# Optimization experiments

Measured on AMD Instinct MI355X. Metric: run time of the kernel, lower is better.

## Reference

```python
import jax, jax.numpy as jnp
import numpy as np

EPS = 1e-12

def _l2_normalize(v, axis):
    norm = jnp.linalg.norm(v, ord=2, axis=axis, keepdims=True)
    return v / jnp.maximum(norm, EPS)

def setup_inputs() -> dict:
    key = jax.random.key(0)
    k1, k2, k3 = jax.random.split(key, 3)
    B, H, W, D, K = 16, 56, 56, 512, 32
    x = jax.random.normal(k1, (B, H, W, D), dtype=jnp.float32)
    # 1x1 conv weight (no bias): equivalent to a (D,K) matmul; he_normal-ish scale
    Wc = jax.random.normal(k2, (D, K), dtype=jnp.float32) * jnp.sqrt(2.0 / D)
    # cluster centers, original shape (1,1,1,512,32) -> stored as (D,K)
    C = jax.random.normal(k3, (D, K), dtype=jnp.float32) * jnp.sqrt(2.0 / D)
    return {"x": x, "Wc": Wc, "C": C}

def reference(x, Wc, C):
    # soft-assignment: 1x1 conv + softmax over clusters
    s = jnp.einsum('bhwd,dk->bhwk', x, Wc)          # (B,H,W,K)
    a = jax.nn.softmax(s, axis=-1)                   # (B,H,W,K)
    # v[b,d,k] = sum_{h,w} a[b,h,w,k] * (x[b,h,w,d] + C[d,k])
    #          = einsum(a,x) + C * sum_{h,w} a   (avoids (B,H,W,D,K) intermediate)
    ax = jnp.einsum('bhwk,bhwd->bdk', a, x)          # (B,D,K)
    a_sum = jnp.sum(a, axis=(1, 2))                  # (B,K)
    v = ax + C[None, :, :] * a_sum[:, None, :]       # (B,D,K)
    # intra-normalize over cluster axis (dim=2), flatten, L2 normalize
    v = _l2_normalize(v, axis=2)
    v = v.reshape(v.shape[0], -1)                    # (B, D*K)
    return _l2_normalize(v, axis=1)
```

## Files before the change

### kernel.cpp

```cpp
#include <hip/hip_runtime.h>
#include <math.h>


#define BATCH 16
#define HW    3136
#define DIM   512
#define KCL   32
#define NCHK  49
#define SLABF (BATCH * DIM * KCL + 256)

typedef __attribute__((ext_vector_type(8))) short short8;
typedef __attribute__((ext_vector_type(4))) float f32x4;

__device__ __forceinline__ void atomAddF(float* p, float v) {
    unsafeAtomicAdd(p, v);
}

__device__ __forceinline__ unsigned short f2bf(float f) {
    unsigned u = __float_as_uint(f);
    return (unsigned short)((u + 0x7FFFu + ((u >> 16) & 1u)) >> 16);
}

__device__ __forceinline__ short8 pack_frag(f32x4 lo, f32x4 hi) {
    union { unsigned short h[8]; short8 s; } r;
    r.h[0] = f2bf(lo[0]); r.h[1] = f2bf(lo[1]); r.h[2] = f2bf(lo[2]); r.h[3] = f2bf(lo[3]);
    r.h[4] = f2bf(hi[0]); r.h[5] = f2bf(hi[1]); r.h[6] = f2bf(hi[2]); r.h[7] = f2bf(hi[3]);
    return r.s;
}

__device__ __forceinline__ f32x4 gload4(const float* p) {
    f32x4 r;
    asm volatile("global_load_dwordx4 %0, %1, off" : "=v"(r) : "v"(p) : "memory");
    return r;
}
__device__ __forceinline__ float gload1(const float* p) {
    float r;
    asm volatile("global_load_dword %0, %1, off" : "=v"(r) : "v"(p) : "memory");
    return r;
}

#define WAITV(N)                                                               \
    do {                                                                       \
        asm volatile("s_waitcnt vmcnt(" #N ")" ::: "memory");                  \
        __builtin_amdgcn_sched_barrier(0);                                     \
    } while (0)

#define WT_STR 520
#define AT_STR 72
#define XT_STR 72

#define P1_TAIL(C, N)                                                          \
    {                                                                          \
        asm volatile("s_waitcnt vmcnt(" #N ")" ::: "memory");                  \
        __builtin_amdgcn_sched_barrier(0);                                     \
        short8 af = pack_frag(afb[(C) & 7][0], afb[(C) & 7][1]);               \
        short8 b0 = *(const short8*)&wt[l15 * WT_STR + (C) * 32 + quad * 8];   \
        short8 b1 = *(const short8*)&wt[(16 + l15) * WT_STR + (C) * 32 + quad * 8]; \
        acc0 = __builtin_amdgcn_mfma_f32_16x16x32_bf16(af, b0, acc0, 0, 0, 0); \
        acc1 = __builtin_amdgcn_mfma_f32_16x16x32_bf16(af, b1, acc1, 0, 0, 0); \
    }

#define LOAD_PF_ASM(PF, DC)                                                    \
    _Pragma("unroll")                                                          \
    for (int i = 0; i < 8; ++i) {                                              \
        const int p = (ph + 2 * i) * 4;                                        \
        _Pragma("unroll")                                                      \
        for (int j = 0; j < 4; ++j)                                            \
            PF[i * 4 + j] = gload1(xc + (size_t)(p + j) * DIM + (DC));         \
    }

#define P2_STAGE(PF)                                                           \
    _Pragma("unroll")                                                          \
    for (int i = 0; i < 8; ++i) {                                              \
        const int p = (ph + 2 * i) * 4;                                        \
        ushort4 w;                                                             \
        w.x = f2bf(PF[i * 4 + 0]); w.y = f2bf(PF[i * 4 + 1]);                  \
        w.z = f2bf(PF[i * 4 + 2]); w.w = f2bf(PF[i * 4 + 3]);                  \
        *(ushort4*)&xt[xtrow * XT_STR + (p ^ xsw)] = w;                        \
    }

#define P2_MFMA_STORE(DC)                                                      \
    {                                                                          \
        f32x4 z = {0.f, 0.f, 0.f, 0.f};                                        \
        f32x4 pacc[2][2];                                                      \
        pacc[0][0] = z; pacc[0][1] = z; pacc[1][0] = z; pacc[1][1] = z;        \
        _Pragma("unroll")                                                      \
        for (int s_ = 0; s_ < 2; ++s_) {                                       \
            const int pb = s_ * 32 + quad * 8;                                 \
            short8 bf0 = *(const short8*)&aT[l15 * AT_STR + pb];               \
            short8 bf1 = *(const short8*)&aT[(16 + l15) * AT_STR + pb];        \
            _Pragma("unroll")                                                  \
            for (int m2 = 0; m2 < 2; ++m2) {                                   \
                const int dloc = wv * 32 + m2 * 16 + l15;                      \
                short8 af = *(const short8*)&xt[dloc * XT_STR + (pb ^ (((dloc >> 3) & 7) << 3))]; \
                pacc[m2][0] = __builtin_amdgcn_mfma_f32_16x16x32_bf16(af, bf0, pacc[m2][0], 0, 0, 0); \
                pacc[m2][1] = __builtin_amdgcn_mfma_f32_16x16x32_bf16(af, bf1, pacc[m2][1], 0, 0, 0); \
            }                                                                  \
        }                                                                      \
        _Pragma("unroll")                                                      \
        for (int m2 = 0; m2 < 2; ++m2) {                                       \
            const int dr = (DC) + (wv * 2 + m2) * 16 + quad * 4;               \
            _Pragma("unroll")                                                  \
            for (int r = 0; r < 4; ++r) {                                      \
                vp[(size_t)(dr + r) * KCL + l15]      = pacc[m2][0][r];        \
                vp[(size_t)(dr + r) * KCL + 16 + l15] = pacc[m2][1][r];        \
            }                                                                  \
        }                                                                      \
    }

__global__ __launch_bounds__(256, 3) void k_sax(const float* __restrict__ x,
                                                const float* __restrict__ Wc,
                                                float* __restrict__ vpart,
                                                float* __restrict__ a_sum) {
    __shared__ __align__(16) unsigned short wt[32 * WT_STR];
    __shared__ __align__(16) unsigned short aT[KCL * AT_STR];
    __shared__ float asum_l[4][32];
    const int t    = threadIdx.x;
    const int lane = t & 63;
    const int wv   = t >> 6;
    const int l15  = lane & 15;
    const int quad = lane >> 4;
    const int n0   = blockIdx.x * 64;
    const int b    = n0 / HW;
    const int ch   = blockIdx.x % NCHK;

    const float* xr = x + (size_t)(n0 + wv * 16 + l15) * DIM + quad * 8;

    f32x4 afb[8][2];
#pragma unroll
    for (int c = 0; c < 8; ++c) {
        afb[c][0] = gload4(xr + c * 32);
        afb[c][1] = gload4(xr + c * 32 + 4);
    }

#pragma unroll
    for (int i = 0; i < 16; ++i) {
        int f  = i * 256 + t;
        int d  = f >> 3;
        int k4 = (f & 7) * 4;
        float4 v = *(const float4*)(Wc + (size_t)d * KCL + k4);
        wt[(k4 + 0) * WT_STR + d] = f2bf(v.x);
        wt[(k4 + 1) * WT_STR + d] = f2bf(v.y);
        wt[(k4 + 2) * WT_STR + d] = f2bf(v.z);
        wt[(k4 + 3) * WT_STR + d] = f2bf(v.w);
    }
    __syncthreads();
    WAITV(0);

    f32x4 acc0 = {0.f, 0.f, 0.f, 0.f};
    f32x4 acc1 = {0.f, 0.f, 0.f, 0.f};
#pragma unroll
    for (int c = 0; c < 8; ++c) {
        short8 af = pack_frag(afb[c][0], afb[c][1]);
        afb[c][0] = gload4(xr + (c + 8) * 32);
        afb[c][1] = gload4(xr + (c + 8) * 32 + 4);
        short8 b0 = *(const short8*)&wt[l15 * WT_STR + c * 32 + quad * 8];
        short8 b1 = *(const short8*)&wt[(16 + l15) * WT_STR + c * 32 + quad * 8];
        acc0 = __builtin_amdgcn_mfma_f32_16x16x32_bf16(af, b0, acc0, 0, 0, 0);
        acc1 = __builtin_amdgcn_mfma_f32_16x16x32_bf16(af, b1, acc1, 0, 0, 0);
    }
    P1_TAIL(8, 14)  P1_TAIL(9, 12)  P1_TAIL(10, 10) P1_TAIL(11, 8)
    P1_TAIL(12, 6)  P1_TAIL(13, 4)  P1_TAIL(14, 2)  P1_TAIL(15, 0)

    float at0 = 0.f, at1 = 0.f;
#pragma unroll
    for (int r = 0; r < 4; ++r) {
        float m = fmaxf(acc0[r], acc1[r]);
        m = fmaxf(m, __shfl_xor(m, 1));
        m = fmaxf(m, __shfl_xor(m, 2));
        m = fmaxf(m, __shfl_xor(m, 4));
        m = fmaxf(m, __shfl_xor(m, 8));
        float e0 = __expf(acc0[r] - m);
        float e1 = __expf(acc1[r] - m);
        float s = e0 + e1;
        s += __shfl_xor(s, 1);
        s += __shfl_xor(s, 2);
        s += __shfl_xor(s, 4);
        s += __shfl_xor(s, 8);
        float inv = 1.f / s;
        float a0 = e0 * inv, a1 = e1 * inv;
        const int pos = wv * 16 + quad * 4 + r;
        aT[l15 * AT_STR + pos]        = f2bf(a0);
        aT[(16 + l15) * AT_STR + pos] = f2bf(a1);
        at0 += a0; at1 += a1;
    }
    at0 += __shfl_xor(at0, 16); at0 += __shfl_xor(at0, 32);
    at1 += __shfl_xor(at1, 16); at1 += __shfl_xor(at1, 32);
    if (quad == 0) {
        asum_l[wv][l15]      = at0;
        asum_l[wv][16 + l15] = at1;
    }

    const int rw    = lane & 31;
    const int ph    = lane >> 5;
    const int xtrow = wv * 32 + rw;
    const int xsw   = ((xtrow >> 3) & 7) << 3;
    unsigned short* xt = wt;
    const float* xc = x + (size_t)n0 * DIM + xtrow;
    float* vp = vpart + (size_t)ch * SLABF + (size_t)b * DIM * KCL;

    float pfA[32], pfB[32];
    LOAD_PF_ASM(pfA, 0);

    __syncthreads();

    WAITV(0);
    LOAD_PF_ASM(pfB, 128);
    P2_STAGE(pfA);
    P2_MFMA_STORE(0);
    LOAD_PF_ASM(pfA, 256);
    WAITV(48);
    P2_STAGE(pfB);
    P2_MFMA_STORE(128);
    LOAD_PF_ASM(pfB, 384);
    WAITV(48);
    P2_STAGE(pfA);
    P2_MFMA_STORE(256);
    WAITV(16);
    P2_STAGE(pfB);
    P2_MFMA_STORE(384);

    if (t < 32)
        atomAddF(&a_sum[b * KCL + t],
                 asum_l[0][t] + asum_l[1][t] + asum_l[2][t] + asum_l[3][t]);
}

__global__ __launch_bounds__(256) void k_norm1(const float* __restrict__ vpart,
                                               const float* __restrict__ a_sum,
                                               const float* __restrict__ Cc,
                                               float* __restrict__ out,
                                               float* __restrict__ ssq) {
    const int t = threadIdx.x;
    const int row = blockIdx.x * 8 + (t >> 5);
    const int k = t & 31;
    const int b = row >> 9;
    const int d = row & 511;

    const float* vp = vpart + (size_t)row * KCL + k;
    float s0 = 0.f, s1 = 0.f, s2 = 0.f, s3 = 0.f;
#pragma unroll
    for (int ps = 0; ps < 48; ps += 4) {
        s0 += vp[(size_t)(ps + 0) * SLABF];
        s1 += vp[(size_t)(ps + 1) * SLABF];
        s2 += vp[(size_t)(ps + 2) * SLABF];
        s3 += vp[(size_t)(ps + 3) * SLABF];
    }
    s0 += vp[(size_t)48 * SLABF];
    float v = (s0 + s1) + (s2 + s3) + Cc[d * KCL + k] * a_sum[b * KCL + k];

    float ss = v * v;
    ss += __shfl_xor(ss, 1, 32);  ss += __shfl_xor(ss, 2, 32);
    ss += __shfl_xor(ss, 4, 32);  ss += __shfl_xor(ss, 8, 32);
    ss += __shfl_xor(ss, 16, 32);
    float inv = 1.f / fmaxf(sqrtf(ss), 1e-12f);
    float r = v * inv;
    out[(size_t)row * KCL + k] = r;

    float bs = r * r;
    for (int off = 32; off > 0; off >>= 1) bs += __shfl_down(bs, off, 64);
    __shared__ float red[4];
    if ((t & 63) == 0) red[t >> 6] = bs;
    __syncthreads();
    if (t == 0) atomAddF(&ssq[b], (red[0] + red[1]) + (red[2] + red[3]));
}

__global__ __launch_bounds__(256) void k_norm2(float* __restrict__ out,
                                               const float* __restrict__ ssq) {
    const int i4 = blockIdx.x * 256 + threadIdx.x;
    const int b = i4 >> 12;
    float inv = 1.f / fmaxf(sqrtf(ssq[b]), 1e-12f);
    float4 v = *(float4*)(out + (size_t)i4 * 4);
    v.x *= inv; v.y *= inv; v.z *= inv; v.w *= inv;
    *(float4*)(out + (size_t)i4 * 4) = v;
}

extern "C" void kernel_launch(void* const* d_in, const int* in_sizes, int n_in,
                              void* d_out, int out_size, void* d_ws, size_t ws_size,
                              hipStream_t stream) {
    const float* x  = (const float*)d_in[0];
    const float* Wc = (const float*)d_in[1];
    const float* Cc = (const float*)d_in[2];
    float* out = (float*)d_out;

    char* ws = (char*)d_ws;
    float* vpart = (float*)ws;
    float* a_sum = (float*)(ws + (size_t)NCHK * SLABF * 4);
    float* ssq   = (float*)(ws + (size_t)NCHK * SLABF * 4 + 2048);

    hipMemsetAsync(a_sum, 0, 2048 + 64, stream);

    k_sax  <<<784, 256, 0, stream>>>(x, Wc, vpart, a_sum);
    k_norm1<<<1024, 256, 0, stream>>>(vpart, a_sum, Cc, out, ssq);
    k_norm2<<<256, 256, 0, stream>>>(out, ssq);
}
```

Baseline: 196.2 us.

## Reuse phase-1 bf16 x fragments in registers instead of reloading x for phase 2

```diff
diff --git a/kernel.cpp b/kernel.cpp
--- a/kernel.cpp
+++ b/kernel.cpp
@@ -33,11 +33,6 @@
     asm volatile("global_load_dwordx4 %0, %1, off" : "=v"(r) : "v"(p) : "memory");
     return r;
 }
-__device__ __forceinline__ float gload1(const float* p) {
-    float r;
-    asm volatile("global_load_dword %0, %1, off" : "=v"(r) : "v"(p) : "memory");
-    return r;
-}
 
 #define WAITV(N)                                                               \
     do {                                                                       \
@@ -45,38 +40,49 @@
         __builtin_amdgcn_sched_barrier(0);                                     \
     } while (0)
 
+#define HBAR()                                                                 \
+    do {                                                                       \
+        __builtin_amdgcn_sched_barrier(0);                                     \
+        asm volatile("s_waitcnt lgkmcnt(0)\n\ts_barrier" ::: "memory");        \
+        __builtin_amdgcn_sched_barrier(0);                                     \
+    } while (0)
+
 #define WT_STR 520
 #define AT_STR 72
 #define XT_STR 72
 
+#define P1_ITER(C)                                                             \
+    {                                                                          \
+        WAITV(14);                                                             \
+        xk[C] = pack_frag(afb[(C) & 7][0], afb[(C) & 7][1]);                   \
+        afb[(C) & 7][0] = gload4(xr + ((C) + 8) * 32);                         \
+        afb[(C) & 7][1] = gload4(xr + ((C) + 8) * 32 + 4);                     \
+        short8 b0 = *(const short8*)&wt[l15 * WT_STR + (C) * 32 + quad * 8];   \
+        short8 b1 = *(const short8*)&wt[(16 + l15) * WT_STR + (C) * 32 + quad * 8]; \
+        acc0 = __builtin_amdgcn_mfma_f32_16x16x32_bf16(xk[C], b0, acc0, 0, 0, 0); \
+        acc1 = __builtin_amdgcn_mfma_f32_16x16x32_bf16(xk[C], b1, acc1, 0, 0, 0); \
+    }
+
 #define P1_TAIL(C, N)                                                          \
     {                                                                          \
         asm volatile("s_waitcnt vmcnt(" #N ")" ::: "memory");                  \
         __builtin_amdgcn_sched_barrier(0);                                     \
-        short8 af = pack_frag(afb[(C) & 7][0], afb[(C) & 7][1]);               \
+        xk[C] = pack_frag(afb[(C) & 7][0], afb[(C) & 7][1]);                   \
         short8 b0 = *(const short8*)&wt[l15 * WT_STR + (C) * 32 + quad * 8];   \
         short8 b1 = *(const short8*)&wt[(16 + l15) * WT_STR + (C) * 32 + quad * 8]; \
-        acc0 = __builtin_amdgcn_mfma_f32_16x16x32_bf16(af, b0, acc0, 0, 0, 0); \
-        acc1 = __builtin_amdgcn_mfma_f32_16x16x32_bf16(af, b1, acc1, 0, 0, 0); \
-    }
-
-#define LOAD_PF_ASM(PF, DC)                                                    \
+        acc0 = __builtin_amdgcn_mfma_f32_16x16x32_bf16(xk[C], b0, acc0, 0, 0, 0); \
+        acc1 = __builtin_amdgcn_mfma_f32_16x16x32_bf16(xk[C], b1, acc1, 0, 0, 0); \
+    }
+
+#define P2_STAGE_REG(DC)                                                       \
     _Pragma("unroll")                                                          \
-    for (int i = 0; i < 8; ++i) {                                              \
-        const int p = (ph + 2 * i) * 4;                                        \
+    for (int cc = 0; cc < 4; ++cc) {                                           \
+        const int swz = ((cc * 4 + quad) & 7) << 3;                            \
+        const int col = (wv * 16 + l15) ^ swz;                                 \
         _Pragma("unroll")                                                      \
-        for (int j = 0; j < 4; ++j)                                            \
-            PF[i * 4 + j] = gload1(xc + (size_t)(p + j) * DIM + (DC));         \
-    }
-
-#define P2_STAGE(PF)                                                           \
-    _Pragma("unroll")                                                          \
-    for (int i = 0; i < 8; ++i) {                                              \
-        const int p = (ph + 2 * i) * 4;                                        \
-        ushort4 w;                                                             \
-        w.x = f2bf(PF[i * 4 + 0]); w.y = f2bf(PF[i * 4 + 1]);                  \
-        w.z = f2bf(PF[i * 4 + 2]); w.w = f2bf(PF[i * 4 + 3]);                  \
-        *(ushort4*)&xt[xtrow * XT_STR + (p ^ xsw)] = w;                        \
+        for (int j = 0; j < 8; ++j)                                            \
+            xt[(cc * 32 + quad * 8 + j) * XT_STR + col] =                      \
+                (unsigned short)xk[(DC) / 32 + cc][j];                         \
     }
 
 #define P2_MFMA_STORE(DC)                                                      \
@@ -144,21 +150,13 @@
         wt[(k4 + 2) * WT_STR + d] = f2bf(v.z);
         wt[(k4 + 3) * WT_STR + d] = f2bf(v.w);
     }
-    __syncthreads();
-    WAITV(0);
-
+    HBAR();
+
+    short8 xk[16];
     f32x4 acc0 = {0.f, 0.f, 0.f, 0.f};
     f32x4 acc1 = {0.f, 0.f, 0.f, 0.f};
-#pragma unroll
-    for (int c = 0; c < 8; ++c) {
-        short8 af = pack_frag(afb[c][0], afb[c][1]);
-        afb[c][0] = gload4(xr + (c + 8) * 32);
-        afb[c][1] = gload4(xr + (c + 8) * 32 + 4);
-        short8 b0 = *(const short8*)&wt[l15 * WT_STR + c * 32 + quad * 8];
-        short8 b1 = *(const short8*)&wt[(16 + l15) * WT_STR + c * 32 + quad * 8];
-        acc0 = __builtin_amdgcn_mfma_f32_16x16x32_bf16(af, b0, acc0, 0, 0, 0);
-        acc1 = __builtin_amdgcn_mfma_f32_16x16x32_bf16(af, b1, acc1, 0, 0, 0);
-    }
+    P1_ITER(0)  P1_ITER(1)  P1_ITER(2)  P1_ITER(3)
+    P1_ITER(4)  P1_ITER(5)  P1_ITER(6)  P1_ITER(7)
     P1_TAIL(8, 14)  P1_TAIL(9, 12)  P1_TAIL(10, 10) P1_TAIL(11, 8)
     P1_TAIL(12, 6)  P1_TAIL(13, 4)  P1_TAIL(14, 2)  P1_TAIL(15, 0)
 
@@ -191,33 +189,25 @@
         asum_l[wv][16 + l15] = at1;
     }
 
-    const int rw    = lane & 31;
-    const int ph    = lane >> 5;
-    const int xtrow = wv * 32 + rw;
-    const int xsw   = ((xtrow >> 3) & 7) << 3;
     unsigned short* xt = wt;
-    const float* xc = x + (size_t)n0 * DIM + xtrow;
     float* vp = vpart + (size_t)ch * SLABF + (size_t)b * DIM * KCL;
 
-    float pfA[32], pfB[32];
-    LOAD_PF_ASM(pfA, 0);
-
     __syncthreads();
 
-    WAITV(0);
-    LOAD_PF_ASM(pfB, 128);
-    P2_STAGE(pfA);
+    P2_STAGE_REG(0);
+    HBAR();
     P2_MFMA_STORE(0);
-    LOAD_PF_ASM(pfA, 256);
-    WAITV(48);
-    P2_STAGE(pfB);
+    HBAR();
+    P2_STAGE_REG(128);
+    HBAR();
     P2_MFMA_STORE(128);
-    LOAD_PF_ASM(pfB, 384);
-    WAITV(48);
-    P2_STAGE(pfA);
+    HBAR();
+    P2_STAGE_REG(256);
+    HBAR();
     P2_MFMA_STORE(256);
-    WAITV(16);
-    P2_STAGE(pfB);
+    HBAR();
+    P2_STAGE_REG(384);
+    HBAR();
     P2_MFMA_STORE(384);
 
     if (t < 32)
```

After: 191.2 us, median of 2. 2.6% less time.
